# Kernel optimization log

Measured on AMD Instinct MI355X. Metric: run time of the kernel, lower is better.

## Reference

```python
import jax, jax.numpy as jnp
import numpy as np

D_MODEL, NUM_HEADS, D_HEAD = 1024, 16, 64
B, T = 2, 2048


def setup_inputs() -> dict:
    key = jax.random.key(0)
    ks = jax.random.split(key, 9)
    s_in = 1.0 / np.sqrt(D_MODEL)
    s_proj = 1.0 / np.sqrt(NUM_HEADS * D_HEAD)
    x = jax.random.normal(ks[0], (B, T, D_MODEL), dtype=jnp.float32)
    # stacked per-head projection weights (nn.Linear: y = x @ W.T + b -> store as [H, C, d_head])
    Wq = jax.random.uniform(ks[1], (NUM_HEADS, D_MODEL, D_HEAD), jnp.float32, -s_in, s_in)
    Wk = jax.random.uniform(ks[2], (NUM_HEADS, D_MODEL, D_HEAD), jnp.float32, -s_in, s_in)
    Wv = jax.random.uniform(ks[3], (NUM_HEADS, D_MODEL, D_HEAD), jnp.float32, -s_in, s_in)
    bq = jax.random.uniform(ks[4], (NUM_HEADS, D_HEAD), jnp.float32, -s_in, s_in)
    bk = jax.random.uniform(ks[5], (NUM_HEADS, D_HEAD), jnp.float32, -s_in, s_in)
    bv = jax.random.uniform(ks[6], (NUM_HEADS, D_HEAD), jnp.float32, -s_in, s_in)
    Wo = jax.random.uniform(ks[7], (NUM_HEADS * D_HEAD, D_MODEL), jnp.float32, -s_proj, s_proj)
    bo = jax.random.uniform(ks[8], (D_MODEL,), jnp.float32, -s_proj, s_proj)
    return {"x": x, "Wq": Wq, "Wk": Wk, "Wv": Wv, "bq": bq, "bk": bk, "bv": bv, "Wo": Wo, "bo": bo}


def reference(x, Wq, Wk, Wv, bq, bk, bv, Wo, bo):
    Bsz, Tlen, C = x.shape
    # per-head projections, vectorized over heads: [B, H, T, d_head]
    q = jnp.einsum('btc,hcd->bhtd', x, Wq) + bq[None, :, None, :]
    k = jnp.einsum('btc,hcd->bhtd', x, Wk) + bk[None, :, None, :]
    v = jnp.einsum('btc,hcd->bhtd', x, Wv) + bv[None, :, None, :]
    # NOTE: source scales by sqrt(C) = sqrt(d_model), not sqrt(d_head); no causal mask
    scores = jnp.einsum('bhtd,bhsd->bhts', q, k) / jnp.sqrt(jnp.asarray(C, x.dtype))
    attn = jax.nn.softmax(scores, axis=-1)
    out = jnp.einsum('bhts,bhsd->bhtd', attn, v)  # [B, H, T, d_head]
    # concat heads along feature dim: [B, T, H*d_head]
    out = jnp.transpose(out, (0, 2, 1, 3)).reshape(Bsz, Tlen, -1)
    return out @ Wo + bo
```

## Files before the change

kernel.cpp:

```cpp
#include <hip/hip_runtime.h>

typedef __bf16 bf16;
typedef __bf16 bf16x4 __attribute__((ext_vector_type(4)));
typedef __bf16 bf16x8 __attribute__((ext_vector_type(8)));
typedef float  f32x4  __attribute__((ext_vector_type(4)));

#define T_SEQ  2048
#define NHEAD  16
#define DHEAD  64
#define DMODEL 1024
#define MTOT   4096
#define L2E    1.4426950408889634f

static __device__ __forceinline__ f32x4 mfma16(bf16x8 a, bf16x8 b, f32x4 c) {
    return __builtin_amdgcn_mfma_f32_16x16x32_bf16(a, b, c, 0, 0, 0);
}

__global__ __launch_bounds__(256) void prep(
    const float* __restrict__ x,  bf16* __restrict__ xbf,
    const float* __restrict__ Wq, const float* __restrict__ Wk,
    const float* __restrict__ Wv, bf16* __restrict__ wt,
    const float* __restrict__ Wo, bf16* __restrict__ wot)
{
    __shared__ float t[64][68];
    const int bid = blockIdx.x, tid = threadIdx.x;

    if (bid < 2048) {
        const int i = bid * 256 + tid;
        const float4 a = ((const float4*)x)[i * 2];
        const float4 b = ((const float4*)x)[i * 2 + 1];
        bf16x8 v;
        v[0] = (bf16)a.x; v[1] = (bf16)a.y; v[2] = (bf16)a.z; v[3] = (bf16)a.w;
        v[4] = (bf16)b.x; v[5] = (bf16)b.y; v[6] = (bf16)b.z; v[7] = (bf16)b.w;
        ((bf16x8*)xbf)[i] = v;
        return;
    }

    const float* in; bf16* out;
    int R, Cc; long ib, ob; int r0, c0;
    if (bid < 2816) {
        int b2 = bid - 2048;
        int w = b2 >> 8, rem = b2 & 255;
        int rt = rem & 15, head = rem >> 4;
        in  = (w == 0 ? Wq : w == 1 ? Wk : Wv);
        out = wt + (size_t)w * 1024 * 1024;
        R = 1024; Cc = 64;
        ib = (long)head * 65536; ob = (long)head * 65536;
        r0 = rt * 64; c0 = 0;
    } else {
        int b3 = bid - 2816;
        in = Wo; out = wot;
        R = 1024; Cc = 1024;
        ib = 0; ob = 0;
        r0 = (b3 & 15) * 64; c0 = (b3 >> 4) * 64;
    }

#pragma unroll
    for (int i = 0; i < 4; ++i) {
        int idx = i * 256 + tid;
        int row = idx >> 4, cb = (idx & 15) * 4;
        float4 v = *(const float4*)&in[ib + (long)(r0 + row) * Cc + c0 + cb];
        t[row][cb + 0] = v.x; t[row][cb + 1] = v.y;
        t[row][cb + 2] = v.z; t[row][cb + 3] = v.w;
    }
    __syncthreads();
#pragma unroll
    for (int i = 0; i < 2; ++i) {
        int idx = i * 256 + tid;
        int row = idx >> 3, cb = (idx & 7) * 8;
        bf16x8 v;
#pragma unroll
        for (int j = 0; j < 8; ++j) v[j] = (bf16)t[cb + j][row];
        *(bf16x8*)&out[ob + (long)(c0 + row) * R + r0 + cb] = v;
    }
}

__global__ __launch_bounds__(256) void qkv_gemm(
    const bf16* __restrict__ x, const bf16* __restrict__ wt,
    const float* __restrict__ bq, const float* __restrict__ bk,
    const float* __restrict__ bv,
    bf16* __restrict__ qws, bf16* __restrict__ kws, bf16* __restrict__ vtws)
{
    __shared__ __align__(16) bf16 xs[128][72];
    __shared__ __align__(16) bf16 wsh[3][64][72];

    const int m0 = blockIdx.x * 128;
    const int h  = blockIdx.y;
    const int tid = threadIdx.x, wid = tid >> 6, lane = tid & 63;
    const int lr = lane & 15, lg = lane >> 4;

    const bf16* wbase[3];
#pragma unroll
    for (int w = 0; w < 3; ++w)
        wbase[w] = wt + ((size_t)(w * NHEAD + h)) * DHEAD * DMODEL;

    f32x4 acc[3][2][4];
#pragma unroll
    for (int w = 0; w < 3; ++w)
#pragma unroll
        for (int mi = 0; mi < 2; ++mi)
#pragma unroll
            for (int nt = 0; nt < 4; ++nt) acc[w][mi][nt] = (f32x4)0.0f;

    bf16x8 xr[4], wr[3][2];
#pragma unroll
    for (int i = 0; i < 4; ++i) {
        int idx = i * 256 + tid;
        int row = idx >> 3, cb = (idx & 7) * 8;
        xr[i] = *(const bf16x8*)&x[(size_t)(m0 + row) * DMODEL + cb];
    }
#pragma unroll
    for (int w = 0; w < 3; ++w)
#pragma unroll
        for (int i = 0; i < 2; ++i) {
            int idx = i * 256 + tid;
            int row = idx >> 3, cb = (idx & 7) * 8;
            wr[w][i] = *(const bf16x8*)&wbase[w][(size_t)row * DMODEL + cb];
        }

    for (int kt = 0; kt < 16; ++kt) {
        __syncthreads();
#pragma unroll
        for (int i = 0; i < 4; ++i) {
            int idx = i * 256 + tid;
            int row = idx >> 3, cb = (idx & 7) * 8;
            *(bf16x8*)&xs[row][cb] = xr[i];
        }
#pragma unroll
        for (int w = 0; w < 3; ++w)
#pragma unroll
            for (int i = 0; i < 2; ++i) {
                int idx = i * 256 + tid;
                int row = idx >> 3, cb = (idx & 7) * 8;
                *(bf16x8*)&wsh[w][row][cb] = wr[w][i];
            }
        __syncthreads();

        if (kt < 15) {
            const int kofs = (kt + 1) * 64;
#pragma unroll
            for (int i = 0; i < 4; ++i) {
                int idx = i * 256 + tid;
                int row = idx >> 3, cb = (idx & 7) * 8;
                xr[i] = *(const bf16x8*)&x[(size_t)(m0 + row) * DMODEL + kofs + cb];
            }
#pragma unroll
            for (int w = 0; w < 3; ++w)
#pragma unroll
                for (int i = 0; i < 2; ++i) {
                    int idx = i * 256 + tid;
                    int row = idx >> 3, cb = (idx & 7) * 8;
                    wr[w][i] = *(const bf16x8*)&wbase[w][(size_t)row * DMODEL + kofs + cb];
                }
        }

        bf16x8 af[2][2];
#pragma unroll
        for (int mi = 0; mi < 2; ++mi)
#pragma unroll
            for (int ks = 0; ks < 2; ++ks)
                af[mi][ks] = *(const bf16x8*)&xs[wid * 32 + mi * 16 + lr][ks * 32 + lg * 8];

#pragma unroll
        for (int w = 0; w < 3; ++w)
#pragma unroll
            for (int nt = 0; nt < 4; ++nt)
#pragma unroll
                for (int ks = 0; ks < 2; ++ks) {
                    bf16x8 bfr = *(const bf16x8*)&wsh[w][nt * 16 + lr][ks * 32 + lg * 8];
#pragma unroll
                    for (int mi = 0; mi < 2; ++mi)
                        acc[w][mi][nt] = mfma16(af[mi][ks], bfr, acc[w][mi][nt]);
                }
    }

    const float* bias[3] = { bq + h * DHEAD, bk + h * DHEAD, bv + h * DHEAD };
#pragma unroll
    for (int w = 0; w < 3; ++w)
#pragma unroll
        for (int nt = 0; nt < 4; ++nt) {
            int d = nt * 16 + lr;
            float bs = bias[w][d];
#pragma unroll
            for (int mi = 0; mi < 2; ++mi)
#pragma unroll
                for (int j = 0; j < 4; ++j) {
                    int mrow = m0 + wid * 32 + mi * 16 + lg * 4 + j;
                    int b = mrow >> 11, t = mrow & 2047;
                    float val = acc[w][mi][nt][j] + bs;
                    size_t bh = (size_t)b * NHEAD + h;
                    if (w == 0)
                        qws[(bh * T_SEQ + t) * DHEAD + d] = (bf16)val;
                    else if (w == 1)
                        kws[(bh * T_SEQ + t) * DHEAD + d] = (bf16)val;
                    else
                        vtws[(bh * DHEAD + d) * T_SEQ + t] = (bf16)val;
                }
        }
}

__global__ __launch_bounds__(512) void attn_fused(
    const bf16* __restrict__ qws, const bf16* __restrict__ kws,
    const bf16* __restrict__ vtws, bf16* __restrict__ aws)
{
    __shared__ __align__(16) bf16 kls[2][64][72];
    __shared__ __align__(16) bf16 vls[2][64][72];
    __shared__ __align__(16) bf16 pls[128][68];

    const int id = blockIdx.x;
    const int w  = (id & 7) * 64 + (id >> 3);
    const int qt = w & 15;
    const int bh = w >> 4;

    const int b = bh >> 4, h = bh & 15;
    const bf16* Q  = qws  + (size_t)bh * T_SEQ * DHEAD;
    const bf16* K  = kws  + (size_t)bh * T_SEQ * DHEAD;
    const bf16* Vt = vtws + (size_t)bh * DHEAD * T_SEQ;

    const int tid = threadIdx.x, wid = tid >> 6, lane = tid & 63;
    const int lr = lane & 15, lg = lane >> 4;
    const int q0 = qt * 128 + wid * 16;

    const int srow = tid >> 3, scb = (tid & 7) * 8;

    bf16x8 qf[2];
#pragma unroll
    for (int ks = 0; ks < 2; ++ks) {
        bf16x8 v = *(const bf16x8*)&Q[(size_t)(q0 + lr) * DHEAD + ks * 32 + lg * 8];
#pragma unroll
        for (int j = 0; j < 8; ++j) v[j] = (bf16)((float)v[j] * 0.03125f);
        qf[ks] = v;
    }

    f32x4 o[4];
#pragma unroll
    for (int nt = 0; nt < 4; ++nt) o[nt] = (f32x4)0.0f;
    float mrun = -1e30f, lrun = 0.f;

    bf16x8 kr, vr;
    kr = *(const bf16x8*)&K[(size_t)srow * DHEAD + scb];
    vr = *(const bf16x8*)&Vt[(size_t)srow * T_SEQ + scb];
    *(bf16x8*)&kls[0][srow][scb] = kr;
    *(bf16x8*)&vls[0][srow][scb] = vr;

    int cur = 0;
    for (int t = 0; t < T_SEQ / 64; ++t) {
        __syncthreads();

        const bool more = (t + 1) < T_SEQ / 64;
        if (more) {
            int kvn = (t + 1) * 64;
            kr = *(const bf16x8*)&K[(size_t)(kvn + srow) * DHEAD + scb];
            vr = *(const bf16x8*)&Vt[(size_t)srow * T_SEQ + kvn + scb];
        }

        f32x4 s[4];
        __builtin_amdgcn_s_setprio(1);
#pragma unroll
        for (int nt = 0; nt < 4; ++nt) {
            bf16x8 k0 = *(const bf16x8*)&kls[cur][nt * 16 + lr][0 + lg * 8];
            bf16x8 k1 = *(const bf16x8*)&kls[cur][nt * 16 + lr][32 + lg * 8];
            s[nt] = mfma16(k0, qf[0], (f32x4)0.0f);
            s[nt] = mfma16(k1, qf[1], s[nt]);
        }
        __builtin_amdgcn_s_setprio(0);

        float vm0 = fmaxf(fmaxf(s[0][0], s[0][1]), fmaxf(s[0][2], s[0][3]));
        float vm1 = fmaxf(fmaxf(s[1][0], s[1][1]), fmaxf(s[1][2], s[1][3]));
        float vm2 = fmaxf(fmaxf(s[2][0], s[2][1]), fmaxf(s[2][2], s[2][3]));
        float vm3 = fmaxf(fmaxf(s[3][0], s[3][1]), fmaxf(s[3][2], s[3][3]));
        float vm = fmaxf(fmaxf(vm0, vm1), fmaxf(vm2, vm3));
        vm = fmaxf(vm, __shfl_xor(vm, 16));
        vm = fmaxf(vm, __shfl_xor(vm, 32));

        const bool skip = __all(vm <= mrun + 8.0f);
        float mnew = skip ? mrun : fmaxf(mrun, vm);
        float m2 = mnew * L2E;

        float p[4][4];
        float rs = 0.f;
#pragma unroll
        for (int nt = 0; nt < 4; ++nt)
#pragma unroll
            for (int j = 0; j < 4; ++j) {
                p[nt][j] = __builtin_amdgcn_exp2f(fmaf(s[nt][j], L2E, -m2));
                rs += p[nt][j];
            }
        rs += __shfl_xor(rs, 16);
        rs += __shfl_xor(rs, 32);

        if (skip) {
            lrun += rs;
        } else {
            float alpha = __builtin_amdgcn_exp2f((mrun - mnew) * L2E);
            lrun = lrun * alpha + rs;
            mrun = mnew;
            float ab[4];
#pragma unroll
            for (int j = 0; j < 4; ++j) ab[j] = __shfl(alpha, lg * 4 + j);
#pragma unroll
            for (int nt = 0; nt < 4; ++nt)
#pragma unroll
                for (int j = 0; j < 4; ++j) o[nt][j] *= ab[j];
        }

#pragma unroll
        for (int nt = 0; nt < 4; ++nt) {
            bf16x4 pk;
            pk[0] = (bf16)p[nt][0]; pk[1] = (bf16)p[nt][1];
            pk[2] = (bf16)p[nt][2]; pk[3] = (bf16)p[nt][3];
            *(bf16x4*)&pls[wid * 16 + lr][nt * 16 + 4 * lg] = pk;
        }

        asm volatile("s_waitcnt lgkmcnt(0)" ::: "memory");

        __builtin_amdgcn_s_setprio(1);
#pragma unroll
        for (int ks = 0; ks < 2; ++ks) {
            bf16x4 ph0 = *(const bf16x4*)&pls[wid * 16 + lr][ks * 32 + lg * 8];
            bf16x4 ph1 = *(const bf16x4*)&pls[wid * 16 + lr][ks * 32 + lg * 8 + 4];
            bf16x8 pf = __builtin_shufflevector(ph0, ph1, 0, 1, 2, 3, 4, 5, 6, 7);
#pragma unroll
            for (int nt = 0; nt < 4; ++nt) {
                bf16x8 vf = *(const bf16x8*)&vls[cur][nt * 16 + lr][ks * 32 + lg * 8];
                o[nt] = mfma16(pf, vf, o[nt]);
            }
        }
        __builtin_amdgcn_s_setprio(0);

        if (more) {
            *(bf16x8*)&kls[cur ^ 1][srow][scb] = kr;
            *(bf16x8*)&vls[cur ^ 1][srow][scb] = vr;
        }
        cur ^= 1;
    }

    float linv[4];
#pragma unroll
    for (int j = 0; j < 4; ++j) linv[j] = 1.0f / __shfl(lrun, lg * 4 + j);

    const size_t obase = ((size_t)b * T_SEQ) * DMODEL + (size_t)h * DHEAD;
#pragma unroll
    for (int nt = 0; nt < 4; ++nt) {
        int d = nt * 16 + lr;
#pragma unroll
        for (int j = 0; j < 4; ++j) {
            int t = q0 + lg * 4 + j;
            aws[obase + (size_t)t * DMODEL + d] = (bf16)(o[nt][j] * linv[j]);
        }
    }
}

__global__ __launch_bounds__(256) void out_gemm(
    const bf16* __restrict__ a, const bf16* __restrict__ wot,
    const float* __restrict__ bo, float* __restrict__ out)
{
    __shared__ __align__(16) bf16 as[128][72];
    __shared__ __align__(16) bf16 wsh[128][72];

    const int m0 = blockIdx.x * 128, n0 = blockIdx.y * 128;
    const int tid = threadIdx.x, wid = tid >> 6, lane = tid & 63;
    const int lr = lane & 15, lg = lane >> 4;

    f32x4 acc[2][8];
#pragma unroll
    for (int mi = 0; mi < 2; ++mi)
#pragma unroll
        for (int nt = 0; nt < 8; ++nt) acc[mi][nt] = (f32x4)0.0f;

    bf16x8 ar[4], wr[4];
#pragma unroll
    for (int i = 0; i < 4; ++i) {
        int idx = i * 256 + tid;
        int row = idx >> 3, cb = (idx & 7) * 8;
        ar[i] = *(const bf16x8*)&a[(size_t)(m0 + row) * DMODEL + cb];
        wr[i] = *(const bf16x8*)&wot[(size_t)(n0 + row) * DMODEL + cb];
    }

    for (int kt = 0; kt < 16; ++kt) {
        __syncthreads();
#pragma unroll
        for (int i = 0; i < 4; ++i) {
            int idx = i * 256 + tid;
            int row = idx >> 3, cb = (idx & 7) * 8;
            *(bf16x8*)&as[row][cb]  = ar[i];
            *(bf16x8*)&wsh[row][cb] = wr[i];
        }
        __syncthreads();

        if (kt < 15) {
            const int kofs = (kt + 1) * 64;
#pragma unroll
            for (int i = 0; i < 4; ++i) {
                int idx = i * 256 + tid;
                int row = idx >> 3, cb = (idx & 7) * 8;
                ar[i] = *(const bf16x8*)&a[(size_t)(m0 + row) * DMODEL + kofs + cb];
                wr[i] = *(const bf16x8*)&wot[(size_t)(n0 + row) * DMODEL + kofs + cb];
            }
        }

        bf16x8 af[2][2];
#pragma unroll
        for (int mi = 0; mi < 2; ++mi)
#pragma unroll
            for (int ks = 0; ks < 2; ++ks)
                af[mi][ks] = *(const bf16x8*)&as[wid * 32 + mi * 16 + lr][ks * 32 + lg * 8];

#pragma unroll
        for (int nt = 0; nt < 8; ++nt)
#pragma unroll
            for (int ks = 0; ks < 2; ++ks) {
                bf16x8 bfr = *(const bf16x8*)&wsh[nt * 16 + lr][ks * 32 + lg * 8];
#pragma unroll
                for (int mi = 0; mi < 2; ++mi)
                    acc[mi][nt] = mfma16(af[mi][ks], bfr, acc[mi][nt]);
            }
    }

#pragma unroll
    for (int nt = 0; nt < 8; ++nt) {
        int n = n0 + nt * 16 + lr;
        float bs = bo[n];
#pragma unroll
        for (int mi = 0; mi < 2; ++mi)
#pragma unroll
            for (int j = 0; j < 4; ++j) {
                int m = m0 + wid * 32 + mi * 16 + lg * 4 + j;
                out[(size_t)m * DMODEL + n] = acc[mi][nt][j] + bs;
            }
    }
}

extern "C" void kernel_launch(void* const* d_in, const int* in_sizes, int n_in,
                              void* d_out, int out_size, void* d_ws, size_t ws_size,
                              hipStream_t stream)
{
    const float* x  = (const float*)d_in[0];
    const float* Wq = (const float*)d_in[1];
    const float* Wk = (const float*)d_in[2];
    const float* Wv = (const float*)d_in[3];
    const float* bq = (const float*)d_in[4];
    const float* bk = (const float*)d_in[5];
    const float* bv = (const float*)d_in[6];
    const float* Wo = (const float*)d_in[7];
    const float* bo = (const float*)d_in[8];
    float* out = (float*)d_out;

    const size_t M1 = (size_t)1024 * 1024;
    bf16* ws   = (bf16*)d_ws;
    bf16* xbf  = ws;
    bf16* qws  = ws + 4 * M1;
    bf16* kws  = qws + 4 * M1;
    bf16* vtws = kws + 4 * M1;
    bf16* wt   = vtws + 4 * M1;
    bf16* wot  = wt + 3 * M1;
    bf16* aws  = xbf;

    dim3 tb(256);
    prep<<<dim3(3072), tb, 0, stream>>>(x, xbf, Wq, Wk, Wv, wt, Wo, wot);
    qkv_gemm<<<dim3(MTOT / 128, NHEAD), tb, 0, stream>>>(xbf, wt, bq, bk, bv, qws, kws, vtws);
    attn_fused<<<dim3(512), dim3(512), 0, stream>>>(qws, kws, vtws, aws);
    out_gemm<<<dim3(MTOT / 128, DMODEL / 128), tb, 0, stream>>>(aws, wot, bo, out);
}
```

Measured before the change: 128.0 us.

## Split attention KV range across blocks and merge partials in combine kernel

Attention is split along the key/value sequence into S chunks (3 or 2, chosen by workspace size), each block writing normalized partial outputs plus running max and sum. A separate combine kernel rescales and merges the partials into the head-concatenated buffer. The goal is more blocks for better CU occupancy and latency hiding. The cost is extra global traffic for the partials, an additional launch, and an extra bf16 rounding step. The per-iteration row-sum shuffle is also moved to after the loop.

```diff
diff --git a/kernel.cpp b/kernel.cpp
--- a/kernel.cpp
+++ b/kernel.cpp
@@ -199,18 +199,23 @@
         }
 }
 
-__global__ __launch_bounds__(512) void attn_fused(
+template<int S, bool PARTIAL>
+__global__ __launch_bounds__(512) void attn_split(
     const bf16* __restrict__ qws, const bf16* __restrict__ kws,
-    const bf16* __restrict__ vtws, bf16* __restrict__ aws)
+    const bf16* __restrict__ vtws,
+    bf16* __restrict__ po, float* __restrict__ pml, bf16* __restrict__ aws)
 {
     __shared__ __align__(16) bf16 kls[2][64][72];
     __shared__ __align__(16) bf16 vls[2][64][72];
     __shared__ __align__(16) bf16 pls[128][68];
 
     const int id = blockIdx.x;
-    const int w  = (id & 7) * 64 + (id >> 3);
-    const int qt = w & 15;
-    const int bh = w >> 4;
+    const int w  = (id & 7) * (64 * S) + (id >> 3);
+    const int bh = w / (16 * S);
+    const int rem = w - bh * (16 * S);
+    const int qt = rem / S;
+    const int sidx = rem - qt * S;
+    const int t0 = (sidx * 32) / S, t1 = ((sidx + 1) * 32) / S;
 
     const int b = bh >> 4, h = bh & 15;
     const bf16* Q  = qws  + (size_t)bh * T_SEQ * DHEAD;
@@ -238,16 +243,16 @@
     float mrun = -1e30f, lrun = 0.f;
 
     bf16x8 kr, vr;
-    kr = *(const bf16x8*)&K[(size_t)srow * DHEAD + scb];
-    vr = *(const bf16x8*)&Vt[(size_t)srow * T_SEQ + scb];
+    kr = *(const bf16x8*)&K[(size_t)(t0 * 64 + srow) * DHEAD + scb];
+    vr = *(const bf16x8*)&Vt[(size_t)srow * T_SEQ + t0 * 64 + scb];
     *(bf16x8*)&kls[0][srow][scb] = kr;
     *(bf16x8*)&vls[0][srow][scb] = vr;
 
     int cur = 0;
-    for (int t = 0; t < T_SEQ / 64; ++t) {
+    for (int t = t0; t < t1; ++t) {
         __syncthreads();
 
-        const bool more = (t + 1) < T_SEQ / 64;
+        const bool more = (t + 1) < t1;
         if (more) {
             int kvn = (t + 1) * 64;
             kr = *(const bf16x8*)&K[(size_t)(kvn + srow) * DHEAD + scb];
@@ -286,8 +291,6 @@
                 p[nt][j] = __builtin_amdgcn_exp2f(fmaf(s[nt][j], L2E, -m2));
                 rs += p[nt][j];
             }
-        rs += __shfl_xor(rs, 16);
-        rs += __shfl_xor(rs, 32);
 
         if (skip) {
             lrun += rs;
@@ -335,20 +338,85 @@
         cur ^= 1;
     }
 
+    float lrow = lrun;
+    lrow += __shfl_xor(lrow, 16);
+    lrow += __shfl_xor(lrow, 32);
+
     float linv[4];
 #pragma unroll
-    for (int j = 0; j < 4; ++j) linv[j] = 1.0f / __shfl(lrun, lg * 4 + j);
-
-    const size_t obase = ((size_t)b * T_SEQ) * DMODEL + (size_t)h * DHEAD;
-#pragma unroll
-    for (int nt = 0; nt < 4; ++nt) {
-        int d = nt * 16 + lr;
-#pragma unroll
-        for (int j = 0; j < 4; ++j) {
-            int t = q0 + lg * 4 + j;
-            aws[obase + (size_t)t * DMODEL + d] = (bf16)(o[nt][j] * linv[j]);
-        }
-    }
+    for (int j = 0; j < 4; ++j) linv[j] = 1.0f / __shfl(lrow, lg * 4 + j);
+
+    if (PARTIAL) {
+        const size_t pbase = (size_t)(sidx * 32 + bh) * T_SEQ * DHEAD;
+#pragma unroll
+        for (int nt = 0; nt < 4; ++nt) {
+            int d = nt * 16 + lr;
+#pragma unroll
+            for (int j = 0; j < 4; ++j) {
+                int tq = q0 + lg * 4 + j;
+                po[pbase + (size_t)tq * DHEAD + d] = (bf16)(o[nt][j] * linv[j]);
+            }
+        }
+        if (lg == 0) {
+            size_t mlidx = ((size_t)(sidx * 32 + bh) * T_SEQ + (q0 + lr)) * 2;
+            pml[mlidx]     = mrun;
+            pml[mlidx + 1] = lrow;
+        }
+    } else {
+        const size_t obase = ((size_t)b * T_SEQ) * DMODEL + (size_t)h * DHEAD;
+#pragma unroll
+        for (int nt = 0; nt < 4; ++nt) {
+            int d = nt * 16 + lr;
+#pragma unroll
+            for (int j = 0; j < 4; ++j) {
+                int tq = q0 + lg * 4 + j;
+                aws[obase + (size_t)tq * DMODEL + d] = (bf16)(o[nt][j] * linv[j]);
+            }
+        }
+    }
+}
+
+template<int S>
+__global__ __launch_bounds__(256) void attn_combine(
+    const bf16* __restrict__ po, const float* __restrict__ pml,
+    bf16* __restrict__ aws)
+{
+    const int g = blockIdx.x * 256 + threadIdx.x;
+    const int r = g >> 3, dblk = g & 7;
+    const int bh = r >> 11, tq = r & 2047;
+
+    float ms[S], ls[S];
+    float m = -1e30f;
+#pragma unroll
+    for (int s = 0; s < S; ++s) {
+        float2 v = ((const float2*)pml)[(size_t)(s * 32 + bh) * T_SEQ + tq];
+        ms[s] = v.x; ls[s] = v.y;
+        m = fmaxf(m, ms[s]);
+    }
+    float L = 0.f, wgt[S];
+#pragma unroll
+    for (int s = 0; s < S; ++s) {
+        wgt[s] = ls[s] * __builtin_amdgcn_exp2f((ms[s] - m) * L2E);
+        L += wgt[s];
+    }
+    float inv = 1.0f / L;
+
+    float acc[8];
+#pragma unroll
+    for (int j = 0; j < 8; ++j) acc[j] = 0.f;
+#pragma unroll
+    for (int s = 0; s < S; ++s) {
+        bf16x8 ov = *(const bf16x8*)&po[((size_t)(s * 32 + bh) * T_SEQ + tq) * DHEAD + dblk * 8];
+        float c = wgt[s] * inv;
+#pragma unroll
+        for (int j = 0; j < 8; ++j) acc[j] = fmaf(c, (float)ov[j], acc[j]);
+    }
+    bf16x8 out;
+#pragma unroll
+    for (int j = 0; j < 8; ++j) out[j] = (bf16)acc[j];
+
+    const int b = bh >> 4, h = bh & 15;
+    *(bf16x8*)&aws[((size_t)(b * T_SEQ + tq)) * DMODEL + h * DHEAD + dblk * 8] = out;
 }
 
 __global__ __launch_bounds__(256) void out_gemm(
@@ -455,10 +523,26 @@
     bf16* wt   = vtws + 4 * M1;
     bf16* wot  = wt + 3 * M1;
     bf16* aws  = xbf;
+    bf16* po   = wot + 1 * M1;
+
+    const size_t BASE = 20 * M1 * 2;
+    const size_t PER  = 4 * M1 * 2 + (size_t)65536 * 2 * 4;
 
     dim3 tb(256);
     prep<<<dim3(3072), tb, 0, stream>>>(x, xbf, Wq, Wk, Wv, wt, Wo, wot);
     qkv_gemm<<<dim3(MTOT / 128, NHEAD), tb, 0, stream>>>(xbf, wt, bq, bk, bv, qws, kws, vtws);
-    attn_fused<<<dim3(512), dim3(512), 0, stream>>>(qws, kws, vtws, aws);
+
+    if (ws_size >= BASE + 3 * PER) {
+        float* pml = (float*)(po + 3 * 4 * M1);
+        attn_split<3, true><<<dim3(1536), dim3(512), 0, stream>>>(qws, kws, vtws, po, pml, aws);
+        attn_combine<3><<<dim3(2048), tb, 0, stream>>>(po, pml, aws);
+    } else if (ws_size >= BASE + 2 * PER) {
+        float* pml = (float*)(po + 2 * 4 * M1);
+        attn_split<2, true><<<dim3(1024), dim3(512), 0, stream>>>(qws, kws, vtws, po, pml, aws);
+        attn_combine<2><<<dim3(2048), tb, 0, stream>>>(po, pml, aws);
+    } else {
+        attn_split<1, false><<<dim3(512), dim3(512), 0, stream>>>(qws, kws, vtws, po, nullptr, aws);
+    }
+
     out_gemm<<<dim3(MTOT / 128, DMODEL / 128), tb, 0, stream>>>(aws, wot, bo, out);
 }
```

Measured after the change: 135.9 us. 6.2% more time.
